# Performance work log

Measured on AMD Instinct MI355X. Metric: run time of the kernel, lower is better.

## Reference

```python
import jax, jax.numpy as jnp
import numpy as np

B, DIM, SIZE = 16, 512, 128

def _conv2d(x, w, pad_h, pad_w):
    # x: [B,C,H,W], w: [O,I,kh,kw]
    return jax.lax.conv_general_dilated(
        x, w, window_strides=(1, 1),
        padding=((pad_h, pad_h), (pad_w, pad_w)),
        dimension_numbers=('NCHW', 'OIHW', 'NCHW'))


def setup_inputs() -> dict:
    key = jax.random.key(0)
    ks = jax.random.split(key, 8)
    s = SIZE
    return {
        'x': jax.random.normal(ks[0], (B, DIM, s, s), dtype=jnp.float32),
        'w_conv': jax.random.normal(ks[1], (2, DIM, 1, 1), dtype=jnp.float32) * (1.0 / np.sqrt(DIM)),
        'w_ww_conv': jax.random.normal(ks[2], (1, 2, s, 5), dtype=jnp.float32) * (1.0 / np.sqrt(2 * s * 5)),
        'w_hw_conv': jax.random.normal(ks[3], (1, 2, 5, s), dtype=jnp.float32) * (1.0 / np.sqrt(2 * s * 5)),
        'ww_lin_w': jax.random.normal(ks[4], (s, s), dtype=jnp.float32) * (1.0 / np.sqrt(s)),
        'ww_lin_b': jax.random.normal(ks[5], (s,), dtype=jnp.float32) * 0.01,
        'hw_lin_w': jax.random.normal(ks[6], (s, s), dtype=jnp.float32) * (1.0 / np.sqrt(s)),
        'hw_lin_b': jax.random.normal(ks[7], (s,), dtype=jnp.float32) * 0.01,
    }


def reference(x, w_conv, w_ww_conv, w_hw_conv, ww_lin_w, ww_lin_b, hw_lin_w, hw_lin_b):
    # 1x1 conv dim -> 2 (no bias, no bn, no act): pure channel GEMM
    x2 = jnp.einsum('bchw,oc->bohw', x, w_conv[:, :, 0, 0])  # [B,2,S,S]

    # ww branch: conv kernel (SIZE,5), pad (0,2) -> [B,1,1,S]
    ww = _conv2d(x2, w_ww_conv, 0, 2)[:, 0, 0, :]            # [B,S]
    ww = jax.nn.sigmoid(ww @ ww_lin_w.T + ww_lin_b)          # Linear + Sigmoid

    # hw branch: conv kernel (5,SIZE), pad (2,0) -> [B,1,S,1]
    hw = _conv2d(x2, w_hw_conv, 2, 0)[:, 0, :, 0]            # [B,S]
    hw = jax.nn.sigmoid(hw @ hw_lin_w.T + hw_lin_b)

    # batched outer product hw (S,1) @ ww (1,S) -> [B,S,S]
    return jnp.einsum('bh,bw->bhw', hw, ww)
```

## Files before the change

kernel.cpp:

```cpp
#include <hip/hip_runtime.h>
#include <math.h>

#define BB   16
#define CC   512
#define SS   128
#define HWSZ (SS * SS)
#define NCH  16
#define CK   (CC / NCH)
#define LP   (SS + 1)

typedef float f4 __attribute__((ext_vector_type(4)));

__global__ __launch_bounds__(1024) void k1a_partial(
    const float* __restrict__ x, const float* __restrict__ wconv,
    float* __restrict__ part)
{
    const int b   = blockIdx.x >> 4;
    const int ck  = blockIdx.x & (NCH - 1);
    const int tid = threadIdx.x;

    const float* xp = x + ((size_t)b * CC + (size_t)ck * CK) * HWSZ + tid * 4;
    const float* wA = wconv + ck * CK;
    const float* wB = wconv + CC + ck * CK;

    f4 a0[4], a1[4];
    #pragma unroll
    for (int s = 0; s < 4; ++s) { a0[s] = (f4)0.f; a1[s] = (f4)0.f; }

    #pragma unroll 4
    for (int c = 0; c < CK; ++c) {
        const float wa = wA[c];
        const float wb = wB[c];
        #pragma unroll
        for (int s = 0; s < 4; ++s) {
            const f4 v = __builtin_nontemporal_load(
                (const f4*)(xp + (size_t)c * HWSZ + s * 4096));
            a0[s].x = fmaf(v.x, wa, a0[s].x);
            a0[s].y = fmaf(v.y, wa, a0[s].y);
            a0[s].z = fmaf(v.z, wa, a0[s].z);
            a0[s].w = fmaf(v.w, wa, a0[s].w);
            a1[s].x = fmaf(v.x, wb, a1[s].x);
            a1[s].y = fmaf(v.y, wb, a1[s].y);
            a1[s].z = fmaf(v.z, wb, a1[s].z);
            a1[s].w = fmaf(v.w, wb, a1[s].w);
        }
    }

    float* pp = part + (size_t)(b * NCH + ck) * 2 * HWSZ + tid * 4;
    #pragma unroll
    for (int s = 0; s < 4; ++s) {
        *(f4*)(pp + s * 4096)        = a0[s];
        *(f4*)(pp + HWSZ + s * 4096) = a1[s];
    }
}

__global__ __launch_bounds__(1024) void k2_rest(
    const float* __restrict__ part,
    const float* __restrict__ wwc,
    const float* __restrict__ hwc,
    const float* __restrict__ wlw, const float* __restrict__ wlb,
    const float* __restrict__ hlw, const float* __restrict__ hlb,
    float* __restrict__ out)
{
    __shared__ float x2l[2][SS][LP];
    __shared__ float tw2[2][2][5][SS];
    __shared__ float uh2[2][2][5][SS];
    __shared__ float vbuf[2 * SS];
    __shared__ float rbuf[2 * SS];

    const int b   = blockIdx.x;
    const int tid = threadIdx.x;

    {
        const float* pb = part + (size_t)b * NCH * 2 * HWSZ;
        #pragma unroll
        for (int it = 0; it < (2 * HWSZ / 4) / 1024; ++it) {
            const int q4 = it * 1024 + tid;
            const int p  = q4 * 4;
            const float* pp = pb + p;
            f4 s = (f4)0.f;
            #pragma unroll
            for (int c = 0; c < NCH; ++c) {
                const f4 v = *(const f4*)(pp + (size_t)c * 2 * HWSZ);
                s.x += v.x; s.y += v.y; s.z += v.z; s.w += v.w;
            }
            const int o   = p >> 14;
            const int pix = p & (HWSZ - 1);
            const int h   = pix >> 7;
            const int w   = pix & (SS - 1);
            x2l[o][h][w + 0] = s.x;
            x2l[o][h][w + 1] = s.y;
            x2l[o][h][w + 2] = s.z;
            x2l[o][h][w + 3] = s.w;
        }
    }
    __syncthreads();

    {
        const int lane = tid & 127;
        const int i    = (tid >> 7) & 1;
        const int br   = (tid >> 8) & 1;
        const int kp   = tid >> 9;
        float acc[5] = {0.f, 0.f, 0.f, 0.f, 0.f};

        if (br == 0) {
            const float* wrow = wwc + i * (SS * 5);
            const int kh0 = kp * 64;
            #pragma unroll 8
            for (int kh = kh0; kh < kh0 + 64; ++kh) {
                const float xv = x2l[i][kh][lane];
                #pragma unroll
                for (int kw = 0; kw < 5; ++kw)
                    acc[kw] = fmaf(xv, wrow[kh * 5 + kw], acc[kw]);
            }
            #pragma unroll
            for (int kw = 0; kw < 5; ++kw) tw2[kp][i][kw][lane] = acc[kw];
        } else {
            const float* wrow = hwc + i * (5 * SS);
            const int kw0 = kp * 64;
            #pragma unroll 8
            for (int kw = kw0; kw < kw0 + 64; ++kw) {
                const float xv = x2l[i][lane][kw];
                #pragma unroll
                for (int kh = 0; kh < 5; ++kh)
                    acc[kh] = fmaf(xv, wrow[kh * SS + kw], acc[kh]);
            }
            #pragma unroll
            for (int kh = 0; kh < 5; ++kh) uh2[kp][i][kh][lane] = acc[kh];
        }
    }
    __syncthreads();

    if (tid < 256) {
        const int pos = tid & 127;
        float s = 0.f;
        if (tid < 128) {
            #pragma unroll
            for (int kw = 0; kw < 5; ++kw) {
                const int wsrc = pos + kw - 2;
                if (wsrc >= 0 && wsrc < SS)
                    s += (tw2[0][0][kw][wsrc] + tw2[0][1][kw][wsrc])
                       + (tw2[1][0][kw][wsrc] + tw2[1][1][kw][wsrc]);
            }
        } else {
            #pragma unroll
            for (int kh = 0; kh < 5; ++kh) {
                const int hsrc = pos + kh - 2;
                if (hsrc >= 0 && hsrc < SS)
                    s += (uh2[0][0][kh][hsrc] + uh2[0][1][kh][hsrc])
                       + (uh2[1][0][kh][hsrc] + uh2[1][1][kh][hsrc]);
            }
        }
        vbuf[tid] = s;
    }
    __syncthreads();

    if (tid < 256) {
        const int j    = tid & 127;
        const int half = tid >> 7;
        const float* lw  = (half == 0) ? wlw : hlw;
        const float* lb  = (half == 0) ? wlb : hlb;
        const float* vin = vbuf + half * SS;
        float s = lb[j];
        const f4* wr = (const f4*)(lw + (size_t)j * SS);
        #pragma unroll 4
        for (int k4 = 0; k4 < SS / 4; ++k4) {
            const f4 wv = wr[k4];
            s = fmaf(vin[4 * k4 + 0], wv.x, s);
            s = fmaf(vin[4 * k4 + 1], wv.y, s);
            s = fmaf(vin[4 * k4 + 2], wv.z, s);
            s = fmaf(vin[4 * k4 + 3], wv.w, s);
        }
        rbuf[tid] = 1.f / (1.f + expf(-s));
    }
    __syncthreads();

    {
        float* ob = out + (size_t)b * HWSZ;
        #pragma unroll
        for (int it = 0; it < (HWSZ / 4) / 1024; ++it) {
            const int p4 = it * 1024 + tid;
            const int h  = p4 >> 5;
            const int w0 = (p4 & 31) * 4;
            const float hv = rbuf[SS + h];
            f4 o;
            o.x = hv * rbuf[w0 + 0];
            o.y = hv * rbuf[w0 + 1];
            o.z = hv * rbuf[w0 + 2];
            o.w = hv * rbuf[w0 + 3];
            *(f4*)(ob + (size_t)h * SS + w0) = o;
        }
    }
}

extern "C" void kernel_launch(void* const* d_in, const int* in_sizes, int n_in,
                              void* d_out, int out_size, void* d_ws, size_t ws_size,
                              hipStream_t stream) {
    const float* x     = (const float*)d_in[0];
    const float* wconv = (const float*)d_in[1];
    const float* wwc   = (const float*)d_in[2];
    const float* hwc   = (const float*)d_in[3];
    const float* wlw   = (const float*)d_in[4];
    const float* wlb   = (const float*)d_in[5];
    const float* hlw   = (const float*)d_in[6];
    const float* hlb   = (const float*)d_in[7];
    float* out = (float*)d_out;

    float* part = (float*)d_ws;

    k1a_partial<<<dim3(BB * NCH), dim3(1024), 0, stream>>>(x, wconv, part);
    k2_rest<<<dim3(BB), dim3(1024), 0, stream>>>(part, wwc, hwc,
                                                 wlw, wlb, hlw, hlb, out);
}
```

Measured before the change: 689.0 us.

## Split channel-GEMM blocks by spatial half and move partial reduction to separate kernel

The first kernel now launches twice as many 512-thread blocks, each covering half the spatial plane, so work is spread more evenly across compute units. The 16-way partial-sum reduction is moved out of the 16-block tail kernel into a new 512-block reduce kernel that writes x2 to workspace. The tail kernel then only loads the reduced x2. This trades one extra launch and an extra x2 round trip through global memory for much wider parallelism in the reduction step.

Result: no change. 681.5 us (-1.1%).

```diff
diff --git a/kernel.cpp b/kernel.cpp
--- a/kernel.cpp
+++ b/kernel.cpp
@@ -11,15 +11,18 @@
 
 typedef float f4 __attribute__((ext_vector_type(4)));
 
-__global__ __launch_bounds__(1024) void k1a_partial(
+__global__ __launch_bounds__(512) void k1a_partial(
     const float* __restrict__ x, const float* __restrict__ wconv,
     float* __restrict__ part)
 {
-    const int b   = blockIdx.x >> 4;
-    const int ck  = blockIdx.x & (NCH - 1);
+    const int b   = blockIdx.x >> 5;
+    const int sub = blockIdx.x & 31;
+    const int ck  = sub >> 1;
+    const int hh  = sub & 1;
     const int tid = threadIdx.x;
 
-    const float* xp = x + ((size_t)b * CC + (size_t)ck * CK) * HWSZ + tid * 4;
+    const float* xp = x + ((size_t)b * CC + (size_t)ck * CK) * HWSZ
+                        + hh * (HWSZ / 2) + tid * 4;
     const float* wA = wconv + ck * CK;
     const float* wB = wconv + CC + ck * CK;
 
@@ -34,7 +37,7 @@
         #pragma unroll
         for (int s = 0; s < 4; ++s) {
             const f4 v = __builtin_nontemporal_load(
-                (const f4*)(xp + (size_t)c * HWSZ + s * 4096));
+                (const f4*)(xp + (size_t)c * HWSZ + s * 2048));
             a0[s].x = fmaf(v.x, wa, a0[s].x);
             a0[s].y = fmaf(v.y, wa, a0[s].y);
             a0[s].z = fmaf(v.z, wa, a0[s].z);
@@ -46,16 +49,37 @@
         }
     }
 
-    float* pp = part + (size_t)(b * NCH + ck) * 2 * HWSZ + tid * 4;
+    float* pp = part + (size_t)(b * NCH + ck) * 2 * HWSZ
+                     + hh * (HWSZ / 2) + tid * 4;
     #pragma unroll
     for (int s = 0; s < 4; ++s) {
-        *(f4*)(pp + s * 4096)        = a0[s];
-        *(f4*)(pp + HWSZ + s * 4096) = a1[s];
-    }
-}
-
-__global__ __launch_bounds__(1024) void k2_rest(
-    const float* __restrict__ part,
+        *(f4*)(pp + s * 2048)        = a0[s];
+        *(f4*)(pp + HWSZ + s * 2048) = a1[s];
+    }
+}
+
+__global__ __launch_bounds__(256) void k1b_reduce(
+    const float* __restrict__ part, float* __restrict__ x2)
+{
+    const int pc  = blockIdx.x & 15;
+    const int o   = (blockIdx.x >> 4) & 1;
+    const int b   = blockIdx.x >> 5;
+    const int tid = threadIdx.x;
+
+    const int p = (pc * 256 + tid) * 4;
+
+    const float* pp = part + ((size_t)(b * NCH) * 2 + o) * HWSZ + p;
+    f4 s = (f4)0.f;
+    #pragma unroll
+    for (int ck = 0; ck < NCH; ++ck) {
+        const f4 v = *(const f4*)(pp + (size_t)ck * 2 * HWSZ);
+        s.x += v.x; s.y += v.y; s.z += v.z; s.w += v.w;
+    }
+    *(f4*)&x2[(size_t)(b * 2 + o) * HWSZ + p] = s;
+}
+
+__global__ __launch_bounds__(1024) void k3_rest(
+    const float* __restrict__ x2g,
     const float* __restrict__ wwc,
     const float* __restrict__ hwc,
     const float* __restrict__ wlw, const float* __restrict__ wlb,
@@ -72,26 +96,19 @@
     const int tid = threadIdx.x;
 
     {
-        const float* pb = part + (size_t)b * NCH * 2 * HWSZ;
+        const float* xb = x2g + (size_t)b * 2 * HWSZ;
         #pragma unroll
         for (int it = 0; it < (2 * HWSZ / 4) / 1024; ++it) {
-            const int q4 = it * 1024 + tid;
-            const int p  = q4 * 4;
-            const float* pp = pb + p;
-            f4 s = (f4)0.f;
-            #pragma unroll
-            for (int c = 0; c < NCH; ++c) {
-                const f4 v = *(const f4*)(pp + (size_t)c * 2 * HWSZ);
-                s.x += v.x; s.y += v.y; s.z += v.z; s.w += v.w;
-            }
+            const int p = (it * 1024 + tid) * 4;
+            const f4 v = *(const f4*)(xb + p);
             const int o   = p >> 14;
             const int pix = p & (HWSZ - 1);
             const int h   = pix >> 7;
             const int w   = pix & (SS - 1);
-            x2l[o][h][w + 0] = s.x;
-            x2l[o][h][w + 1] = s.y;
-            x2l[o][h][w + 2] = s.z;
-            x2l[o][h][w + 3] = s.w;
+            x2l[o][h][w + 0] = v.x;
+            x2l[o][h][w + 1] = v.y;
+            x2l[o][h][w + 2] = v.z;
+            x2l[o][h][w + 3] = v.w;
         }
     }
     __syncthreads();
@@ -207,8 +224,10 @@
     float* out = (float*)d_out;
 
     float* part = (float*)d_ws;
-
-    k1a_partial<<<dim3(BB * NCH), dim3(1024), 0, stream>>>(x, wconv, part);
-    k2_rest<<<dim3(BB), dim3(1024), 0, stream>>>(part, wwc, hwc,
+    float* x2   = part + (size_t)BB * NCH * 2 * HWSZ;
+
+    k1a_partial<<<dim3(BB * NCH * 2), dim3(512), 0, stream>>>(x, wconv, part);
+    k1b_reduce<<<dim3(BB * 2 * 16), dim3(256), 0, stream>>>(part, x2);
+    k3_rest<<<dim3(BB), dim3(1024), 0, stream>>>(x2, wwc, hwc,
                                                  wlw, wlb, hlw, hlb, out);
 }
```
